# Kernel optimization log

Hardware: AMD Instinct MI355X
Metric: run time of the kernel (lower is better)

The kernel has to match this reference:

```python
import jax, jax.numpy as jnp
import numpy as np

N_GRAPHS = 200
NODES_PER_GRAPH = 500
N_NODES = N_GRAPHS * NODES_PER_GRAPH  # 100000
N_EDGES = 1_600_000
INPUT_DIM = 64
GCN_DIM = 128
SEQ_LEN = 20
LSTM_DIM = 128
OUTPUT_DIM = 1


def setup_inputs() -> dict:
    key = jax.random.key(0)
    ks = jax.random.split(key, 10)
    # edges constrained to stay inside each graph (block-diagonal adjacency)
    src = jax.random.randint(ks[0], (N_EDGES,), 0, N_NODES, dtype=jnp.int32)
    dst_local = jax.random.randint(ks[1], (N_EDGES,), 0, NODES_PER_GRAPH, dtype=jnp.int32)
    dst = (src // NODES_PER_GRAPH) * NODES_PER_GRAPH + dst_local
    graph_ids = jnp.arange(N_NODES, dtype=jnp.int32) // NODES_PER_GRAPH
    x = jax.random.normal(ks[2], (N_NODES, INPUT_DIM), dtype=jnp.float32)
    s = 0.05
    w_gcn = jax.random.normal(ks[3], (INPUT_DIM, GCN_DIM), dtype=jnp.float32) * s
    b_gcn = jnp.zeros((GCN_DIM,), dtype=jnp.float32)
    w_ih = jax.random.normal(ks[4], (4 * LSTM_DIM, GCN_DIM), dtype=jnp.float32) * s
    w_hh = jax.random.normal(ks[5], (4 * LSTM_DIM, LSTM_DIM), dtype=jnp.float32) * s
    b_ih = jax.random.normal(ks[6], (4 * LSTM_DIM,), dtype=jnp.float32) * s
    b_hh = jax.random.normal(ks[7], (4 * LSTM_DIM,), dtype=jnp.float32) * s
    w_fc = jax.random.normal(ks[8], (OUTPUT_DIM, LSTM_DIM), dtype=jnp.float32) * s
    b_fc = jnp.zeros((OUTPUT_DIM,), dtype=jnp.float32)
    return {"x": x, "src": src, "dst": dst, "graph_ids": graph_ids,
            "w_gcn": w_gcn, "b_gcn": b_gcn, "w_ih": w_ih, "w_hh": w_hh,
            "b_ih": b_ih, "b_hh": b_hh, "w_fc": w_fc, "b_fc": b_fc}


def reference(x, src, dst, graph_ids, w_gcn, b_gcn, w_ih, w_hh, b_ih, b_hh, w_fc, b_fc):
    ones_e = jnp.ones((src.shape[0],), dtype=x.dtype)
    # DGL GraphConv norm='both': D_out^{-1/2} on src side, D_in^{-1/2} on dst side,
    # degrees clamped to min 1 (allow_zero_in_degree=True)
    out_deg = jnp.clip(jax.ops.segment_sum(ones_e, src, num_segments=N_NODES), 1.0)
    in_deg = jnp.clip(jax.ops.segment_sum(ones_e, dst, num_segments=N_NODES), 1.0)
    h = x * (out_deg ** -0.5)[:, None]                               # [N, Din]
    agg = jax.ops.segment_sum(h[src], dst, num_segments=N_NODES)     # gather+scatter-add
    h = agg * (in_deg ** -0.5)[:, None]
    h = jnp.maximum(h @ w_gcn + b_gcn, 0.0)                           # [N, GCN_DIM], ReLU
    # dgl.mean_nodes: per-graph mean pool
    cnt = jax.ops.segment_sum(jnp.ones((N_NODES,), h.dtype), graph_ids, num_segments=N_GRAPHS)
    hg = jax.ops.segment_sum(h, graph_ids, num_segments=N_GRAPHS) / cnt[:, None]  # [T, D]
    # build_dataset: sliding windows of length SEQ_LEN over the graph time series
    B = N_GRAPHS - SEQ_LEN + 1
    idx = jnp.arange(B)[:, None] + jnp.arange(SEQ_LEN)[None, :]
    dat = hg[idx]                                                      # [B, L, D]
    # single-layer LSTM (PyTorch gate order i,f,g,o), zero initial state
    x_proj = jnp.einsum('bld,gd->blg', dat, w_ih) + b_ih               # [B, L, 4H]
    h0 = jnp.zeros((B, LSTM_DIM), dat.dtype)
    c0 = jnp.zeros((B, LSTM_DIM), dat.dtype)

    def step(carry, xt):
        hprev, cprev = carry
        gates = xt + hprev @ w_hh.T + b_hh
        i, f, g, o = jnp.split(gates, 4, axis=-1)
        c = jax.nn.sigmoid(f) * cprev + jax.nn.sigmoid(i) * jnp.tanh(g)
        hh = jax.nn.sigmoid(o) * jnp.tanh(c)
        return (hh, c), None

    (h_n, _), _ = jax.lax.scan(step, (h0, c0), jnp.swapaxes(x_proj, 0, 1))
    pred = h_n @ w_fc.T + b_fc                                         # [B, OUTPUT_DIM]
    return pred
```

## Files before the change

### kernel.cpp

```cpp
#include <hip/hip_runtime.h>
#include <hip/hip_bf16.h>

#define N_GRAPHS 200
#define NPG      500
#define NPGP     512
#define N_NODES_ 100000
#define N_EDGES_ 1600000
#define DIN      64
#define DG       128
#define SEQ      20
#define HL       128
#define G4       512
#define BWIN     (N_GRAPHS - SEQ + 1)
#define NPART    512
#define EPB      (N_EDGES_/NPART)
#define SLOTS    48
#define CAP      9216

typedef __attribute__((ext_vector_type(8))) short short8;
typedef __attribute__((ext_vector_type(4))) float float4v;
typedef __attribute__((ext_vector_type(2))) _Float16 half2v;

__device__ __forceinline__ float sigmoidf_(float v){ return 1.0f/(1.0f+expf(-v)); }

__device__ __forceinline__ unsigned short f2bf(float f) {
  unsigned int u = __float_as_uint(f);
  u += 0x7fffu + ((u >> 16) & 1u);
  return (unsigned short)(u >> 16);
}

__device__ __forceinline__ float h2dot(half2v a, half2v b, float c) {
#if __has_builtin(__builtin_amdgcn_fdot2)
  return __builtin_amdgcn_fdot2(a, b, c, false);
#else
  return c + (float)a.x*(float)b.x + (float)a.y*(float)b.y;
#endif
}

__global__ __launch_bounds__(256) void k_part(const int* __restrict__ src,
                                              const int* __restrict__ dst,
                                              const float* __restrict__ w_hh,
                                              int* __restrict__ gcount,
                                              int* __restrict__ part,
                                              int4* __restrict__ whh16) {
  __shared__ int cnt[N_GRAPHS];
  __shared__ int base[N_GRAPHS];
  __shared__ int buf[N_GRAPHS][SLOTS];
  int b = blockIdx.x, t = threadIdx.x;
  if (b < 32) {
    int i = b*256 + t;
    int k4 = i >> 9, r = i & 511;
    const float4* wp = (const float4*)(w_hh + (size_t)r*HL + k4*8);
    float4 w0 = wp[0], w1 = wp[1];
    half2v p0 = {(_Float16)w0.x, (_Float16)w0.y};
    half2v p1 = {(_Float16)w0.z, (_Float16)w0.w};
    half2v p2 = {(_Float16)w1.x, (_Float16)w1.y};
    half2v p3 = {(_Float16)w1.z, (_Float16)w1.w};
    int4 pk;
    pk.x = __builtin_bit_cast(int, p0); pk.y = __builtin_bit_cast(int, p1);
    pk.z = __builtin_bit_cast(int, p2); pk.w = __builtin_bit_cast(int, p3);
    whh16[i] = pk;
  }
  for (int g = t; g < N_GRAPHS; g += 256) cnt[g] = 0;
  __syncthreads();
  int e0 = b*EPB;
  for (int i = t; i < EPB; i += 256) {
    int s = src[e0+i], d = dst[e0+i];
    int g = s / NPG;
    int pk = ((s - g*NPG) << 9) | (d - g*NPG);
    int pos = atomicAdd(&cnt[g], 1);
    if (pos < SLOTS) buf[g][pos] = pk;
    else { int gp = atomicAdd(&gcount[g], 1); part[g*CAP + gp] = pk; }
  }
  __syncthreads();
  if (t < N_GRAPHS) base[t] = atomicAdd(&gcount[t], min(cnt[t], SLOTS));
  __syncthreads();
  int w = t >> 6, lane = t & 63;
  for (int g = w; g < N_GRAPHS; g += 4) {
    int n = min(cnt[g], SLOTS);
    if (lane < n) part[g*CAP + base[g] + lane] = buf[g][lane];
  }
}

__global__ __launch_bounds__(512, 1) void k_graph(
    const int* __restrict__ gcount, const int* __restrict__ part,
    const float* __restrict__ x,
    const float* __restrict__ w_gcn, const float* __restrict__ b_gcn,
    const float* __restrict__ w_ih,  const float* __restrict__ b_ih,
    float* __restrict__ proj) {
  __shared__ int indeg[512];
  __shared__ int outdeg[512];
  __shared__ int off[512];
  __shared__ float soS[512];
  __shared__ int wsum[8];
  __shared__ float fpS[2];
  __shared__ unsigned short sorted[CAP];
  __shared__ __align__(16) int4 xs[4008];
  __shared__ __align__(16) int4 hpre[4096];
  int g = blockIdx.x, t = threadIdx.x;
  int lane = t & 63, w = t >> 6;

  float4 wg[4];
  #pragma unroll
  for (int q = 0; q < 4; ++q) wg[q] = ((const float4*)w_gcn)[t + q*512];

  indeg[t] = 0; outdeg[t] = 0;
  __syncthreads();
  int nseg = gcount[g], seg0 = g*CAP;
  for (int e = t; e < nseg; e += 512) {
    int p = part[seg0 + e];
    atomicAdd(&indeg[p & 511], 1);
    atomicAdd(&outdeg[p >> 9], 1);
  }
  __syncthreads();
  int v = indeg[t], sc = v;
  #pragma unroll
  for (int o = 1; o < 64; o <<= 1) { int nn = __shfl_up(sc, o); if (lane >= o) sc += nn; }
  if (lane == 63) wsum[w] = sc;
  __syncthreads();
  int woff = 0;
  #pragma unroll
  for (int i = 0; i < 8; ++i) woff += (i < w) ? wsum[i] : 0;
  off[t] = woff + sc - v;
  soS[t] = rsqrtf((float)max(outdeg[t], 1));
  __syncthreads();
  const float4* xg = ((const float4*)x) + (size_t)g*8000;
  ushort4* xd = (ushort4*)xs;
  for (int i = t; i < 8000; i += 512) {
    float4 vv = xg[i];
    float s2 = soS[i >> 4];
    ushort4 u;
    u.x = f2bf(vv.x*s2); u.y = f2bf(vv.y*s2); u.z = f2bf(vv.z*s2); u.w = f2bf(vv.w*s2);
    xd[i] = u;
  }
  if (t < 16) xd[8000 + t] = make_ushort4(0,0,0,0);
  for (int e = t; e < nseg; e += 512) {
    int p = part[seg0 + e];
    int pos = atomicAdd(&off[p & 511], 1);
    sorted[pos] = (unsigned short)(p >> 9);
  }
  __syncthreads();
  int g8 = lane >> 3, fl = lane & 7;
  int G = w*8 + g8;
  for (int sI = 0; sI < 8; ++sI) {
    int nl = sI*64 + G;
    int4 outv = make_int4(0,0,0,0);
    if (nl < NPG) {
      int end = off[nl], dgr = indeg[nl], st = end - dgr;
      float aHi[4] = {0.f,0.f,0.f,0.f};
      float aLo[4] = {0.f,0.f,0.f,0.f};
      int ev = (fl < dgr) ? (int)sorted[st + fl] : 500;
      for (int c0 = 0; c0 < dgr; c0 += 8) {
        int nc = c0 + 8;
        int evn = (nc + fl < dgr) ? (int)sorted[st + nc + fl] : 500;
        #pragma unroll
        for (int j = 0; j < 8; ++j) {
          int se = __shfl(ev, (g8 << 3) + j);
          int4 vv = xs[(se << 3) + fl];
          aHi[0] += __uint_as_float((unsigned)vv.x & 0xffff0000u);
          aLo[0] += __uint_as_float((unsigned)vv.x << 16);
          aHi[1] += __uint_as_float((unsigned)vv.y & 0xffff0000u);
          aLo[1] += __uint_as_float((unsigned)vv.y << 16);
          aHi[2] += __uint_as_float((unsigned)vv.z & 0xffff0000u);
          aLo[2] += __uint_as_float((unsigned)vv.z << 16);
          aHi[3] += __uint_as_float((unsigned)vv.w & 0xffff0000u);
          aLo[3] += __uint_as_float((unsigned)vv.w << 16);
        }
        ev = evn;
      }
      float sn = rsqrtf((float)max(dgr, 1));
      outv.x = (int)(((unsigned)f2bf(aLo[0]*sn)) | ((unsigned)f2bf(aHi[0]*sn) << 16));
      outv.y = (int)(((unsigned)f2bf(aLo[1]*sn)) | ((unsigned)f2bf(aHi[1]*sn) << 16));
      outv.z = (int)(((unsigned)f2bf(aLo[2]*sn)) | ((unsigned)f2bf(aHi[2]*sn) << 16));
      outv.w = (int)(((unsigned)f2bf(aLo[3]*sn)) | ((unsigned)f2bf(aHi[3]*sn) << 16));
    }
    hpre[(nl << 3) + (fl ^ (nl & 7))] = outv;
  }
  __syncthreads();
  unsigned short* wLds = (unsigned short*)sorted;
  #pragma unroll
  for (int q = 0; q < 4; ++q) {
    int i = t + q*512;
    int k = i >> 5, c4 = (i & 31) << 2;
    int h = k >> 5, j = k & 7, lhi = ((k >> 3) & 3) << 4;
    float vvv[4] = {wg[q].x, wg[q].y, wg[q].z, wg[q].w};
    #pragma unroll
    for (int u = 0; u < 4; ++u) {
      int n = c4 + u;
      int idx = ((n >> 4)*2 + h)*64 + lhi + (n & 15);
      wLds[idx*8 + j] = f2bf(vvv[u]);
    }
  }
  __syncthreads();
  float* pS  = (float*)indeg;
  float* hgS = (float*)off;
  int quad = lane >> 4, l15 = lane & 15;
  float bcol[8];
  #pragma unroll
  for (int nt = 0; nt < 8; ++nt) bcol[nt] = b_gcn[nt*16 + l15];
  float psum[8] = {0.f,0.f,0.f,0.f,0.f,0.f,0.f,0.f};
  for (int i = 0; i < 4; ++i) {
    int row0 = (w + 8*i) << 4;
    int r = row0 + l15;
    int4 a0i = hpre[(r << 3) + (quad ^ (r & 7))];
    int4 a1i = hpre[(r << 3) + ((quad + 4) ^ (r & 7))];
    short8 a0 = *(const short8*)&a0i;
    short8 a1 = *(const short8*)&a1i;
    #pragma unroll
    for (int nt = 0; nt < 8; ++nt) {
      short8 b0 = *((const short8*)&wLds[((nt*2+0)*64 + lane)*8]);
      short8 b1 = *((const short8*)&wLds[((nt*2+1)*64 + lane)*8]);
      float4v acc = {0.f, 0.f, 0.f, 0.f};
      acc = __builtin_amdgcn_mfma_f32_16x16x32_bf16(a0, b0, acc, 0, 0, 0);
      acc = __builtin_amdgcn_mfma_f32_16x16x32_bf16(a1, b1, acc, 0, 0, 0);
      #pragma unroll
      for (int r4 = 0; r4 < 4; ++r4) {
        int node = row0 + quad*4 + r4;
        float vvv = acc[r4] + bcol[nt];
        psum[nt] += (node < NPG) ? fmaxf(vvv, 0.f) : 0.f;
      }
    }
  }
  #pragma unroll
  for (int nt = 0; nt < 8; ++nt) {
    float vvv = psum[nt];
    vvv += __shfl_xor(vvv, 16);
    vvv += __shfl_xor(vvv, 32);
    if (lane < 16) pS[w*DG + nt*16 + lane] = vvv;
  }
  __syncthreads();
  if (t < DG) {
    float sum = 0.f;
    #pragma unroll
    for (int w8 = 0; w8 < 8; ++w8) sum += pS[w8*DG + t];
    hgS[t] = sum * (1.0f/NPG);
  }
  __syncthreads();
  const float4* wr = (const float4*)(w_ih + (size_t)t*HL);
  const float4* hv = (const float4*)hgS;
  float acc = b_ih[t];
  #pragma unroll
  for (int k4 = 0; k4 < 32; ++k4) {
    float4 w4 = wr[k4]; float4 h4 = hv[k4];
    acc += w4.x*h4.x + w4.y*h4.y + w4.z*h4.z + w4.w*h4.w;
  }
  proj[(size_t)g*G4 + t] = acc;
  (void)fpS;
}

__global__ __launch_bounds__(512) void k_lstm(const float* __restrict__ proj,
    const int4* __restrict__ whh16, const float* __restrict__ b_hh,
    const float* __restrict__ w_fc, const float* __restrict__ b_fc,
    float* __restrict__ out) {
  __shared__ float gS[G4];
  __shared__ __align__(16) int4 hPi[16];
  __shared__ float fcS[2];
  int b = blockIdx.x, t = threadIdx.x;
  int4 W[16];
  #pragma unroll
  for (int k4 = 0; k4 < 16; ++k4) W[k4] = whh16[(k4 << 9) + t];
  if (t < 16) hPi[t] = make_int4(0,0,0,0);
  float bh = b_hh[t];
  float c = 0.f;
  __syncthreads();
  for (int l = 0; l < SEQ; ++l) {
    float a0 = proj[(size_t)(b+l)*G4 + t] + bh;
    float a1 = 0.f, a2 = 0.f, a3 = 0.f;
    #pragma unroll
    for (int k4 = 0; k4 < 16; k4 += 4) {
      int4 hv0 = hPi[k4+0]; int4 hv1 = hPi[k4+1];
      int4 hv2 = hPi[k4+2]; int4 hv3 = hPi[k4+3];
      a0 = h2dot(__builtin_bit_cast(half2v, W[k4+0].x), __builtin_bit_cast(half2v, hv0.x), a0);
      a0 = h2dot(__builtin_bit_cast(half2v, W[k4+0].y), __builtin_bit_cast(half2v, hv0.y), a0);
      a0 = h2dot(__builtin_bit_cast(half2v, W[k4+0].z), __builtin_bit_cast(half2v, hv0.z), a0);
      a0 = h2dot(__builtin_bit_cast(half2v, W[k4+0].w), __builtin_bit_cast(half2v, hv0.w), a0);
      a1 = h2dot(__builtin_bit_cast(half2v, W[k4+1].x), __builtin_bit_cast(half2v, hv1.x), a1);
      a1 = h2dot(__builtin_bit_cast(half2v, W[k4+1].y), __builtin_bit_cast(half2v, hv1.y), a1);
      a1 = h2dot(__builtin_bit_cast(half2v, W[k4+1].z), __builtin_bit_cast(half2v, hv1.z), a1);
      a1 = h2dot(__builtin_bit_cast(half2v, W[k4+1].w), __builtin_bit_cast(half2v, hv1.w), a1);
      a2 = h2dot(__builtin_bit_cast(half2v, W[k4+2].x), __builtin_bit_cast(half2v, hv2.x), a2);
      a2 = h2dot(__builtin_bit_cast(half2v, W[k4+2].y), __builtin_bit_cast(half2v, hv2.y), a2);
      a2 = h2dot(__builtin_bit_cast(half2v, W[k4+2].z), __builtin_bit_cast(half2v, hv2.z), a2);
      a2 = h2dot(__builtin_bit_cast(half2v, W[k4+2].w), __builtin_bit_cast(half2v, hv2.w), a2);
      a3 = h2dot(__builtin_bit_cast(half2v, W[k4+3].x), __builtin_bit_cast(half2v, hv3.x), a3);
      a3 = h2dot(__builtin_bit_cast(half2v, W[k4+3].y), __builtin_bit_cast(half2v, hv3.y), a3);
      a3 = h2dot(__builtin_bit_cast(half2v, W[k4+3].z), __builtin_bit_cast(half2v, hv3.z), a3);
      a3 = h2dot(__builtin_bit_cast(half2v, W[k4+3].w), __builtin_bit_cast(half2v, hv3.w), a3);
    }
    gS[t] = (a0 + a1) + (a2 + a3);
    __syncthreads();
    if (t < 128) {
      float iv = sigmoidf_(gS[t]);
      float fv = sigmoidf_(gS[HL + t]);
      float gv = tanhf(gS[2*HL + t]);
      float ov = sigmoidf_(gS[3*HL + t]);
      c = fv*c + iv*gv;
      float h = ov * tanhf(c);
      float hp2 = __shfl_xor(h, 1);
      if (!(t & 1)) {
        half2v hp = {(_Float16)h, (_Float16)hp2};
        ((int*)hPi)[t >> 1] = __builtin_bit_cast(int, hp);
      }
      if (l == SEQ-1) {
        float s = h * w_fc[t];
        #pragma unroll
        for (int o = 32; o > 0; o >>= 1) s += __shfl_down(s, o);
        if ((t & 63) == 0) fcS[t >> 6] = s;
      }
    }
    __syncthreads();
  }
  if (t == 0) out[b] = fcS[0] + fcS[1] + b_fc[0];
}

extern "C" void kernel_launch(void* const* d_in, const int* in_sizes, int n_in,
                              void* d_out, int out_size, void* d_ws, size_t ws_size,
                              hipStream_t stream) {
  const float* x     = (const float*)d_in[0];
  const int*   src   = (const int*)d_in[1];
  const int*   dst   = (const int*)d_in[2];
  const float* w_gcn = (const float*)d_in[4];
  const float* b_gcn = (const float*)d_in[5];
  const float* w_ih  = (const float*)d_in[6];
  const float* w_hh  = (const float*)d_in[7];
  const float* b_ih  = (const float*)d_in[8];
  const float* b_hh  = (const float*)d_in[9];
  const float* w_fc  = (const float*)d_in[10];
  const float* b_fc  = (const float*)d_in[11];
  float* out = (float*)d_out;

  char* ws = (char*)d_ws;
  size_t off = 0;
  auto alloc = [&](size_t bytes) -> void* {
    void* p = ws + off; off += (bytes + 255) & ~(size_t)255; return p;
  };
  int* gcount  = (int*)alloc((size_t)N_GRAPHS*4);
  int* part    = (int*)alloc((size_t)N_GRAPHS*CAP*4);
  int4* whh16  = (int4*)alloc((size_t)8192*16);
  float* proj  = (float*)alloc((size_t)N_GRAPHS*G4*4);
  (void)ws_size; (void)in_sizes; (void)n_in; (void)out_size;

  hipMemsetAsync(gcount, 0, (size_t)N_GRAPHS*4, stream);
  k_part<<<NPART, 256, 0, stream>>>(src, dst, w_hh, gcount, part, whh16);
  k_graph<<<N_GRAPHS, 512, 0, stream>>>(gcount, part, x, w_gcn, b_gcn, w_ih, b_ih, proj);
  k_lstm<<<BWIN, 512, 0, stream>>>(proj, whh16, b_hh, w_fc, b_fc, out);
}
```

Before: 182.6 us.

## Run per-graph kernel with 1024 threads and cache edge records in registers

The per-graph kernel now launches 1024 threads instead of 512. All stages are remapped to match: degree counting, x scaling, neighbour aggregation over 4 node slices, MFMA row tiles over 16 waves, and the w_ih projection split across thread pairs joined by a shuffle. Each thread loads its partition entries into registers once and reuses them for both the degree count and the sort pass, instead of reading global memory twice. Since only 200 blocks run, one per CU, the aim is more waves per CU to hide LDS and global latency. The cost is higher register pressure and a branch-dependent barrier in the prefix-scan stage.

Result: faster. 171.4 us (-6.1%).

```diff
diff --git a/kernel.cpp b/kernel.cpp
--- a/kernel.cpp
+++ b/kernel.cpp
@@ -82,51 +82,65 @@
   }
 }
 
-__global__ __launch_bounds__(512, 1) void k_graph(
+__global__ __launch_bounds__(1024) void k_graph(
     const int* __restrict__ gcount, const int* __restrict__ part,
     const float* __restrict__ x,
     const float* __restrict__ w_gcn, const float* __restrict__ b_gcn,
     const float* __restrict__ w_ih,  const float* __restrict__ b_ih,
     float* __restrict__ proj) {
-  __shared__ int indeg[512];
-  __shared__ int outdeg[512];
-  __shared__ int off[512];
-  __shared__ float soS[512];
+  __shared__ int meta[2048];
   __shared__ int wsum[8];
-  __shared__ float fpS[2];
+  __shared__ __align__(16) float hgS[DG];
   __shared__ unsigned short sorted[CAP];
   __shared__ __align__(16) int4 xs[4008];
   __shared__ __align__(16) int4 hpre[4096];
+  int* indeg  = meta;
+  int* outdeg = meta + 512;
+  int* off    = meta + 1024;
+  float* soS  = (float*)(meta + 1536);
   int g = blockIdx.x, t = threadIdx.x;
   int lane = t & 63, w = t >> 6;
 
-  float4 wg[4];
-  #pragma unroll
-  for (int q = 0; q < 4; ++q) wg[q] = ((const float4*)w_gcn)[t + q*512];
-
-  indeg[t] = 0; outdeg[t] = 0;
+  float4 wg[2];
+  #pragma unroll
+  for (int q = 0; q < 2; ++q) wg[q] = ((const float4*)w_gcn)[t + q*1024];
+
+  meta[t] = 0; meta[t + 1024] = 0;
   __syncthreads();
   int nseg = gcount[g], seg0 = g*CAP;
-  for (int e = t; e < nseg; e += 512) {
-    int p = part[seg0 + e];
-    atomicAdd(&indeg[p & 511], 1);
-    atomicAdd(&outdeg[p >> 9], 1);
-  }
-  __syncthreads();
-  int v = indeg[t], sc = v;
-  #pragma unroll
-  for (int o = 1; o < 64; o <<= 1) { int nn = __shfl_up(sc, o); if (lane >= o) sc += nn; }
-  if (lane == 63) wsum[w] = sc;
-  __syncthreads();
-  int woff = 0;
-  #pragma unroll
-  for (int i = 0; i < 8; ++i) woff += (i < w) ? wsum[i] : 0;
-  off[t] = woff + sc - v;
-  soS[t] = rsqrtf((float)max(outdeg[t], 1));
+  int pr[9];
+  #pragma unroll
+  for (int q = 0; q < 9; ++q) {
+    int e = t + q*1024;
+    pr[q] = (e < nseg) ? part[seg0 + e] : -1;
+  }
+  #pragma unroll
+  for (int q = 0; q < 9; ++q) {
+    int p = pr[q];
+    if (p >= 0) {
+      atomicAdd(&indeg[p & 511], 1);
+      atomicAdd(&outdeg[p >> 9], 1);
+    }
+  }
+  __syncthreads();
+  if (t < 512) {
+    int v = indeg[t], sc = v;
+    #pragma unroll
+    for (int o = 1; o < 64; o <<= 1) { int nn = __shfl_up(sc, o); if (lane >= o) sc += nn; }
+    if (lane == 63) wsum[t >> 6] = sc;
+    __syncthreads();
+    int woff = 0;
+    #pragma unroll
+    for (int i = 0; i < 8; ++i) woff += (i < (t >> 6)) ? wsum[i] : 0;
+    off[t] = woff + sc - v;
+    soS[t] = rsqrtf((float)max(outdeg[t], 1));
+  } else {
+    __syncthreads();
+  }
   __syncthreads();
   const float4* xg = ((const float4*)x) + (size_t)g*8000;
   ushort4* xd = (ushort4*)xs;
-  for (int i = t; i < 8000; i += 512) {
+  for (int i = t; i < 8000; i += 1024) {
     float4 vv = xg[i];
     float s2 = soS[i >> 4];
     ushort4 u;
@@ -134,16 +148,19 @@
     xd[i] = u;
   }
   if (t < 16) xd[8000 + t] = make_ushort4(0,0,0,0);
-  for (int e = t; e < nseg; e += 512) {
-    int p = part[seg0 + e];
-    int pos = atomicAdd(&off[p & 511], 1);
-    sorted[pos] = (unsigned short)(p >> 9);
+  #pragma unroll
+  for (int q = 0; q < 9; ++q) {
+    int p = pr[q];
+    if (p >= 0) {
+      int pos = atomicAdd(&off[p & 511], 1);
+      sorted[pos] = (unsigned short)(p >> 9);
+    }
   }
   __syncthreads();
   int g8 = lane >> 3, fl = lane & 7;
   int G = w*8 + g8;
-  for (int sI = 0; sI < 8; ++sI) {
-    int nl = sI*64 + G;
+  for (int sI = 0; sI < 4; ++sI) {
+    int nl = sI*128 + G;
     int4 outv = make_int4(0,0,0,0);
     if (nl < NPG) {
       int end = off[nl], dgr = indeg[nl], st = end - dgr;
@@ -179,8 +196,8 @@
   __syncthreads();
   unsigned short* wLds = (unsigned short*)sorted;
   #pragma unroll
-  for (int q = 0; q < 4; ++q) {
-    int i = t + q*512;
+  for (int q = 0; q < 2; ++q) {
+    int i = t + q*1024;
     int k = i >> 5, c4 = (i & 31) << 2;
     int h = k >> 5, j = k & 7, lhi = ((k >> 3) & 3) << 4;
     float vvv[4] = {wg[q].x, wg[q].y, wg[q].z, wg[q].w};
@@ -192,15 +209,15 @@
     }
   }
   __syncthreads();
-  float* pS  = (float*)indeg;
-  float* hgS = (float*)off;
+  float* pS = (float*)meta;
   int quad = lane >> 4, l15 = lane & 15;
   float bcol[8];
   #pragma unroll
   for (int nt = 0; nt < 8; ++nt) bcol[nt] = b_gcn[nt*16 + l15];
   float psum[8] = {0.f,0.f,0.f,0.f,0.f,0.f,0.f,0.f};
-  for (int i = 0; i < 4; ++i) {
-    int row0 = (w + 8*i) << 4;
+  #pragma unroll
+  for (int i = 0; i < 2; ++i) {
+    int row0 = (w + 16*i) << 4;
     int r = row0 + l15;
     int4 a0i = hpre[(r << 3) + (quad ^ (r & 7))];
     int4 a1i = hpre[(r << 3) + ((quad + 4) ^ (r & 7))];
@@ -232,20 +249,23 @@
   if (t < DG) {
     float sum = 0.f;
     #pragma unroll
-    for (int w8 = 0; w8 < 8; ++w8) sum += pS[w8*DG + t];
+    for (int w16 = 0; w16 < 16; ++w16) sum += pS[w16*DG + t];
     hgS[t] = sum * (1.0f/NPG);
   }
   __syncthreads();
-  const float4* wr = (const float4*)(w_ih + (size_t)t*HL);
-  const float4* hv = (const float4*)hgS;
-  float acc = b_ih[t];
-  #pragma unroll
-  for (int k4 = 0; k4 < 32; ++k4) {
-    float4 w4 = wr[k4]; float4 h4 = hv[k4];
-    acc += w4.x*h4.x + w4.y*h4.y + w4.z*h4.z + w4.w*h4.w;
-  }
-  proj[(size_t)g*G4 + t] = acc;
-  (void)fpS;
+  {
+    int r = t >> 1, half = t & 1;
+    const float4* wr = (const float4*)(w_ih + (size_t)r*HL) + half*16;
+    const float4* hv = (const float4*)hgS + half*16;
+    float acc = half ? 0.f : b_ih[r];
+    #pragma unroll
+    for (int k4 = 0; k4 < 16; ++k4) {
+      float4 w4 = wr[k4]; float4 h4 = hv[k4];
+      acc += w4.x*h4.x + w4.y*h4.y + w4.z*h4.z + w4.w*h4.w;
+    }
+    acc += __shfl_xor(acc, 1);
+    if (!half) proj[(size_t)g*G4 + r] = acc;
+  }
 }
 
 __global__ __launch_bounds__(512) void k_lstm(const float* __restrict__ proj,
@@ -342,6 +362,6 @@
 
   hipMemsetAsync(gcount, 0, (size_t)N_GRAPHS*4, stream);
   k_part<<<NPART, 256, 0, stream>>>(src, dst, w_hh, gcount, part, whh16);
-  k_graph<<<N_GRAPHS, 512, 0, stream>>>(gcount, part, x, w_gcn, b_gcn, w_ih, b_ih, proj);
+  k_graph<<<N_GRAPHS, 1024, 0, stream>>>(gcount, part, x, w_gcn, b_gcn, w_ih, b_ih, proj);
   k_lstm<<<BWIN, 512, 0, stream>>>(proj, whh16, b_hh, w_fc, b_fc, out);
 }
```
